# Kernel tuning notes

Hardware: AMD Instinct MI355X
Metric: run time of the kernel (lower is better)

## Reference

```python
import jax, jax.numpy as jnp
import numpy as np

N = 10000       # nodes
E = 320000      # edges
D = 256         # feature dim (out_channels)
L = 5           # num_layers


def setup_inputs() -> dict:
    key = jax.random.key(0)
    ks = jax.random.split(key, 8)
    x = jax.random.normal(ks[0], (N, D), dtype=jnp.float32)
    edge_index = jax.random.randint(ks[1], (2, E), 0, N, dtype=jnp.int64)
    edge_attr = jax.random.uniform(ks[2], (E,), dtype=jnp.float32)
    s = 1.0 / np.sqrt(D)
    # per-layer message transform weights [L, D, D]
    weight = jax.random.uniform(ks[3], (L, D, D), minval=-s, maxval=s, dtype=jnp.float32)
    # GRUCell parameters (torch layout: [3D, D] rows = r, z, n)
    w_ih = jax.random.uniform(ks[4], (3 * D, D), minval=-s, maxval=s, dtype=jnp.float32)
    w_hh = jax.random.uniform(ks[5], (3 * D, D), minval=-s, maxval=s, dtype=jnp.float32)
    b_ih = jax.random.uniform(ks[6], (3 * D,), minval=-s, maxval=s, dtype=jnp.float32)
    b_hh = jax.random.uniform(ks[7], (3 * D,), minval=-s, maxval=s, dtype=jnp.float32)
    return {"x": x, "edge_index": edge_index, "edge_attr": edge_attr,
            "weight": weight, "w_ih": w_ih, "w_hh": w_hh,
            "b_ih": b_ih, "b_hh": b_hh}


def _gru_cell(inp, h, w_ih, w_hh, b_ih, b_hh):
    # torch.nn.GRUCell math
    gi = inp @ w_ih.T + b_ih    # [N, 3D]
    gh = h @ w_hh.T + b_hh      # [N, 3D]
    i_r, i_z, i_n = jnp.split(gi, 3, axis=-1)
    h_r, h_z, h_n = jnp.split(gh, 3, axis=-1)
    r = jax.nn.sigmoid(i_r + h_r)
    z = jax.nn.sigmoid(i_z + h_z)
    n = jnp.tanh(i_n + r * h_n)
    return (1.0 - z) * n + z * h


def reference(x, edge_index, edge_attr, weight, w_ih, w_hh, b_ih, b_hh):
    src, dst = edge_index[0], edge_index[1]
    h = x
    for l in range(L):
        m = h @ weight[l]                                   # [N, D]
        msg = m[src] * edge_attr[:, None]                   # [E, D]
        agg = jax.ops.segment_sum(msg, dst, num_segments=N)  # [N, D]
        h = _gru_cell(agg, h, w_ih, w_hh, b_ih, b_hh)
    return h
```

## Files before the change

kernel.cpp:

```cpp
#include <hip/hip_runtime.h>
#include <hip/hip_bf16.h>

#define NN 10000
#define NPAD 10048
#define EE 320000
#define DD 256
#define LL 5

typedef __bf16 bf16x8 __attribute__((ext_vector_type(8)));
typedef float f32x4 __attribute__((ext_vector_type(4)));

__device__ __forceinline__ void gload_lds16(const void* g, void* l) {
    __builtin_amdgcn_global_load_lds(
        (const __attribute__((address_space(1))) void*)g,
        (__attribute__((address_space(3))) void*)l, 16, 0, 0);
}


__global__ void transpose_wb_k(const float* __restrict__ W, __bf16* __restrict__ Wt) {
    __shared__ float t[32][33];
    int l = blockIdx.z;
    int bx = blockIdx.x * 32;
    int by = blockIdx.y * 32;
    for (int i = threadIdx.y; i < 32; i += 8)
        t[i][threadIdx.x] = W[l * 65536 + (by + i) * DD + bx + threadIdx.x];
    __syncthreads();
    for (int i = threadIdx.y; i < 32; i += 8)
        Wt[l * 65536 + (bx + i) * DD + by + threadIdx.x] = (__bf16)t[threadIdx.x][i];
}

__global__ void prep_k(const float* __restrict__ w_ih, const float* __restrict__ w_hh,
                       const float* __restrict__ x,
                       __bf16* __restrict__ wihb, __bf16* __restrict__ whhb,
                       float* __restrict__ hb, __bf16* __restrict__ hbfA,
                       __bf16* __restrict__ hbfB, __bf16* __restrict__ mb,
                       __bf16* __restrict__ aggb, int* __restrict__ deg) {
    int i = blockIdx.x * blockDim.x + threadIdx.x;
    if (i < NN * DD) { float v = x[i]; hb[i] = v; hbfA[i] = (__bf16)v; }
    if (i < 768 * 256) { wihb[i] = (__bf16)w_ih[i]; whhb[i] = (__bf16)w_hh[i]; }
    if (i < (NPAD - NN) * DD) {
        hbfA[NN * DD + i] = (__bf16)0.f;
        hbfB[NN * DD + i] = (__bf16)0.f;
        mb[NN * DD + i] = (__bf16)0.f;
        aggb[NN * DD + i] = (__bf16)0.f;
    }
    if (i < NN) deg[i] = 0;
}

__global__ void hist_k(const int* __restrict__ dst, int* __restrict__ deg) {
    int e = blockIdx.x * blockDim.x + threadIdx.x;
    if (e < EE) atomicAdd(&deg[dst[e]], 1);
}

__global__ void scan_k(const int* __restrict__ deg, int* __restrict__ row_start,
                       int* __restrict__ cursor) {
    __shared__ int sums[1024];
    const int CH = 10;
    int t = threadIdx.x;
    int base = t * CH;
    int loc[CH];
    int s = 0;
#pragma unroll
    for (int i = 0; i < CH; i++) {
        int v = (base + i < NN) ? deg[base + i] : 0;
        loc[i] = s;
        s += v;
    }
    sums[t] = s;
    __syncthreads();
    for (int off = 1; off < 1024; off <<= 1) {
        int v = (t >= off) ? sums[t - off] : 0;
        __syncthreads();
        sums[t] += v;
        __syncthreads();
    }
    int pre = (t == 0) ? 0 : sums[t - 1];
#pragma unroll
    for (int i = 0; i < CH; i++) {
        int idx = base + i;
        if (idx < NN) {
            int v = pre + loc[i];
            row_start[idx] = v;
            cursor[idx] = v;
        }
    }
    if (t == 1023) row_start[NN] = sums[1023];
}

__global__ void fill_k(const int* __restrict__ ei, const float* __restrict__ attr,
                       int* __restrict__ cursor, int* __restrict__ ssrc,
                       float* __restrict__ sattr) {
    int e = blockIdx.x * blockDim.x + threadIdx.x;
    if (e < EE) {
        int dv = ei[EE + e];
        int p = atomicAdd(&cursor[dv], 1);
        ssrc[p] = ei[e];
        sattr[p] = attr[e];
    }
}


__global__ __launch_bounds__(256, 2)
void gemm_m_k(const __bf16* __restrict__ hbf, const __bf16* __restrict__ wt,
              __bf16* __restrict__ mout) {
    __shared__ __bf16 sA[2][64][32];
    __shared__ __bf16 sB[2][64][32];
    int tid = threadIdx.x;
    int wave = tid >> 6, lane = tid & 63;
    int ln = lane & 15, quad = lane >> 4;
    int rowBlock = blockIdx.x * 64;
    int colBlock = blockIdx.y * 64;
    int rowHalf = (wave >> 1) * 32;
    int colHalf = (wave & 1) * 32;
    int r4 = lane >> 2;
    int kb = (lane & 3) * 8;

    f32x4 acc[2][2] = {};

    for (int k0 = 0; k0 < DD; k0 += 64) {
        __syncthreads();
#pragma unroll
        for (int ii = 0; ii < 4; ii++) {
            int idx = wave * 4 + ii;
            int mat = idx >> 3;
            int rem = idx & 7;
            int sub = rem >> 2;
            int rg = rem & 3;
            const __bf16* src;
            __bf16* dst;
            if (mat == 0) {
                src = hbf + (size_t)(rowBlock + rg * 16 + r4) * DD + k0 + sub * 32 + kb;
                dst = &sA[sub][rg * 16][0];
            } else {
                src = wt + (size_t)(colBlock + rg * 16 + r4) * DD + k0 + sub * 32 + kb;
                dst = &sB[sub][rg * 16][0];
            }
            gload_lds16(src, dst);
        }
        __syncthreads();

#pragma unroll
        for (int sub = 0; sub < 2; sub++) {
            bf16x8 af[2], bf[2];
#pragma unroll
            for (int i = 0; i < 2; i++)
                af[i] = *(const bf16x8*)&sA[sub][rowHalf + i * 16 + ln][quad * 8];
#pragma unroll
            for (int cc = 0; cc < 2; cc++)
                bf[cc] = *(const bf16x8*)&sB[sub][colHalf + cc * 16 + ln][quad * 8];
#pragma unroll
            for (int nf = 0; nf < 2; nf++)
#pragma unroll
                for (int cc = 0; cc < 2; cc++)
                    acc[nf][cc] = __builtin_amdgcn_mfma_f32_16x16x32_bf16(af[nf], bf[cc], acc[nf][cc], 0, 0, 0);
        }
    }
#pragma unroll
    for (int nf = 0; nf < 2; nf++)
#pragma unroll
        for (int r = 0; r < 4; r++) {
            int n = rowBlock + rowHalf + nf * 16 + quad * 4 + r;
#pragma unroll
            for (int cc = 0; cc < 2; cc++) {
                int d = colBlock + colHalf + cc * 16 + ln;
                mout[(size_t)n * DD + d] = (__bf16)acc[nf][cc][r];
            }
        }
}


__global__ __launch_bounds__(256)
void aggregate_bf_k(const __bf16* __restrict__ m, const int* __restrict__ row_start,
                    const int* __restrict__ ssrc, const float* __restrict__ sattr,
                    __bf16* __restrict__ aggb) {
    __shared__ int sIdx[4][64];
    __shared__ float sAtt[4][64];
    int w = threadIdx.x >> 6, lane = threadIdx.x & 63;
    int n = blockIdx.x * 4 + w;
    int s0 = row_start[n], s1 = row_start[n + 1];
    int half = lane >> 5;
    int c8 = (lane & 31) * 8;

    float acc[8] = {0.f, 0.f, 0.f, 0.f, 0.f, 0.f, 0.f, 0.f};

    for (int base = s0; base < s1; base += 64) {
        int cnt = min(64, s1 - base);
        if (lane < cnt) {
            sIdx[w][lane] = ssrc[base + lane];
            sAtt[w][lane] = sattr[base + lane];
        }
        int t = 0;
        for (; t + 8 <= cnt; t += 8) {
#pragma unroll
            for (int u = 0; u < 4; u++) {
                int e = t + u * 2 + half;
                int s = sIdx[w][e];
                float ww = sAtt[w][e];
                bf16x8 v = *(const bf16x8*)(m + (size_t)s * DD + c8);
#pragma unroll
                for (int i = 0; i < 8; i++) acc[i] += (float)v[i] * ww;
            }
        }
        for (; t + 2 <= cnt; t += 2) {
            int e = t + half;
            int s = sIdx[w][e];
            float ww = sAtt[w][e];
            bf16x8 v = *(const bf16x8*)(m + (size_t)s * DD + c8);
#pragma unroll
            for (int i = 0; i < 8; i++) acc[i] += (float)v[i] * ww;
        }
        if (t < cnt && half == 0) {
            int s = sIdx[w][t];
            float ww = sAtt[w][t];
            bf16x8 v = *(const bf16x8*)(m + (size_t)s * DD + c8);
#pragma unroll
            for (int i = 0; i < 8; i++) acc[i] += (float)v[i] * ww;
        }
    }

#pragma unroll
    for (int i = 0; i < 8; i++) acc[i] += __shfl_xor(acc[i], 32, 64);

    if (half == 0) {
        bf16x8 o;
#pragma unroll
        for (int i = 0; i < 8; i++) o[i] = (__bf16)acc[i];
        *(bf16x8*)(aggb + (size_t)n * DD + c8) = o;
    }
}


__global__ __launch_bounds__(256, 2)
void gru_mfma_k(const __bf16* __restrict__ aggb, const __bf16* __restrict__ hbf,
                const float* __restrict__ hin,
                const __bf16* __restrict__ wih, const __bf16* __restrict__ whh,
                const float* __restrict__ b_ih, const float* __restrict__ b_hh,
                float* __restrict__ hout, __bf16* __restrict__ hbfout) {
    __shared__ __bf16 sA[2][64][32];
    __shared__ __bf16 sB[6][64][32];
    int tid = threadIdx.x;
    int wave = tid >> 6, lane = tid & 63;
    int ln = lane & 15, quad = lane >> 4;
    int nodeBlock = blockIdx.x * 64;
    int colBlock = blockIdx.y * 64;
    int nodeHalf = (wave >> 1) * 32;
    int colHalf = (wave & 1) * 32;
    int r4 = lane >> 2;
    int kb = (lane & 3) * 8;

    f32x4 acc[6][2][2] = {};

    for (int k0 = 0; k0 < DD; k0 += 32) {
        __syncthreads();
#pragma unroll
        for (int ii = 0; ii < 8; ii++) {
            int idx = wave * 8 + ii;
            const __bf16* src;
            __bf16* dst;
            if (idx < 8) {
                int s = idx >> 2;
                int rg = idx & 3;
                const __bf16* A = s ? hbf : aggb;
                src = A + (size_t)(nodeBlock + rg * 16 + r4) * DD + k0 + kb;
                dst = &sA[s][rg * 16][0];
            } else {
                int j = idx - 8;
                int g6 = j >> 2;
                int rg = j & 3;
                const __bf16* B = (g6 < 3) ? wih : whh;
                int brow = (g6 % 3) * 256 + colBlock + rg * 16 + r4;
                src = B + (size_t)brow * DD + k0 + kb;
                dst = &sB[g6][rg * 16][0];
            }
            gload_lds16(src, dst);
        }
        __syncthreads();

        bf16x8 aA[2], aH[2];
#pragma unroll
        for (int nf = 0; nf < 2; nf++) {
            aA[nf] = *(const bf16x8*)&sA[0][nodeHalf + nf * 16 + ln][quad * 8];
            aH[nf] = *(const bf16x8*)&sA[1][nodeHalf + nf * 16 + ln][quad * 8];
        }
#pragma unroll
        for (int g = 0; g < 3; g++) {
#pragma unroll
            for (int cc = 0; cc < 2; cc++) {
                bf16x8 bI = *(const bf16x8*)&sB[g][colHalf + cc * 16 + ln][quad * 8];
                bf16x8 bH = *(const bf16x8*)&sB[3 + g][colHalf + cc * 16 + ln][quad * 8];
#pragma unroll
                for (int nf = 0; nf < 2; nf++) {
                    acc[g][nf][cc] = __builtin_amdgcn_mfma_f32_16x16x32_bf16(aA[nf], bI, acc[g][nf][cc], 0, 0, 0);
                    acc[3 + g][nf][cc] = __builtin_amdgcn_mfma_f32_16x16x32_bf16(aH[nf], bH, acc[3 + g][nf][cc], 0, 0, 0);
                }
            }
        }
    }

#pragma unroll
    for (int nf = 0; nf < 2; nf++) {
#pragma unroll
        for (int r = 0; r < 4; r++) {
            int n = nodeBlock + nodeHalf + nf * 16 + quad * 4 + r;
            if (n >= NN) continue;
#pragma unroll
            for (int cc = 0; cc < 2; cc++) {
                int d = colBlock + colHalf + cc * 16 + ln;
                float ir = acc[0][nf][cc][r] + b_ih[d];
                float iz = acc[1][nf][cc][r] + b_ih[d + 256];
                float in_ = acc[2][nf][cc][r] + b_ih[d + 512];
                float hr = acc[3][nf][cc][r] + b_hh[d];
                float hz = acc[4][nf][cc][r] + b_hh[d + 256];
                float hn = acc[5][nf][cc][r] + b_hh[d + 512];
                float rr = 1.f / (1.f + __expf(-(ir + hr)));
                float zz = 1.f / (1.f + __expf(-(iz + hz)));
                float ax = in_ + rr * hn;
                float e2 = __expf(-2.f * ax);
                float nnv = 2.f / (1.f + e2) - 1.f;
                float hp = hin[(size_t)n * DD + d];
                float o = (1.f - zz) * nnv + zz * hp;
                hout[(size_t)n * DD + d] = o;
                hbfout[(size_t)n * DD + d] = (__bf16)o;
            }
        }
    }
}


extern "C" void kernel_launch(void* const* d_in, const int* in_sizes, int n_in,
                              void* d_out, int out_size, void* d_ws, size_t ws_size,
                              hipStream_t stream) {
    const float* x = (const float*)d_in[0];
    const int* edge_index = (const int*)d_in[1];
    const float* edge_attr = (const float*)d_in[2];
    const float* weight = (const float*)d_in[3];
    const float* w_ih = (const float*)d_in[4];
    const float* w_hh = (const float*)d_in[5];
    const float* b_ih = (const float*)d_in[6];
    const float* b_hh = (const float*)d_in[7];

    size_t off = 0;
    char* base = (char*)d_ws;
    auto carve = [&](size_t bytes) -> void* {
        void* p = base + off;
        off += (bytes + 255) & ~(size_t)255;
        return p;
    };
    float* hb = (float*)carve((size_t)NPAD * DD * 4);
    __bf16* hbfA = (__bf16*)carve((size_t)NPAD * DD * 2);
    __bf16* hbfB = (__bf16*)carve((size_t)NPAD * DD * 2);
    __bf16* mb = (__bf16*)carve((size_t)NPAD * DD * 2);
    __bf16* aggb = (__bf16*)carve((size_t)NPAD * DD * 2);
    __bf16* wtb = (__bf16*)carve((size_t)LL * DD * DD * 2);
    __bf16* wihb = (__bf16*)carve((size_t)768 * DD * 2);
    __bf16* whhb = (__bf16*)carve((size_t)768 * DD * 2);
    int* deg = (int*)carve((size_t)NN * 4);
    int* row_start = (int*)carve((size_t)(NN + 1) * 4);
    int* cursor = (int*)carve((size_t)NN * 4);
    int* ssrc = (int*)carve((size_t)EE * 4);
    float* sattr = (float*)carve((size_t)EE * 4);
    (void)ws_size;

    transpose_wb_k<<<dim3(8, 8, LL), dim3(32, 8), 0, stream>>>(weight, wtb);
    prep_k<<<(NN * DD + 255) / 256, 256, 0, stream>>>(w_ih, w_hh, x, wihb, whhb,
                                                      hb, hbfA, hbfB, mb, aggb, deg);
    hist_k<<<(EE + 255) / 256, 256, 0, stream>>>(edge_index + EE, deg);
    scan_k<<<1, 1024, 0, stream>>>(deg, row_start, cursor);
    fill_k<<<(EE + 255) / 256, 256, 0, stream>>>(edge_index, edge_attr, cursor, ssrc, sattr);

    float* hA = hb;
    float* hB = (float*)d_out;
    __bf16* hbfIn = hbfA;
    __bf16* hbfOut = hbfB;
    for (int l = 0; l < LL; l++) {
        gemm_m_k<<<dim3(157, 4), 256, 0, stream>>>(hbfIn, wtb + (size_t)l * DD * DD, mb);
        aggregate_bf_k<<<2500, 256, 0, stream>>>(mb, row_start, ssrc, sattr, aggb);
        gru_mfma_k<<<dim3(157, 4), 256, 0, stream>>>(aggb, hbfIn, hA, wihb, whhb,
                                                     b_ih, b_hh, hB, hbfOut);
        float* t = hA; hA = hB; hB = t;
        __bf16* tb = hbfIn; hbfIn = hbfOut; hbfOut = tb;
    }
}
```

Before: 371.5 us.

## Fold per-layer message weight into GRU input weights, drop message GEMM

Uses linearity: segment_sum((h@W_l)[src]*a) @ W_ih^T equals segment_sum(h[src]*a) @ (W_ih W_l^T)^T, so a fused weight W_ih·W_l^T is precomputed once per layer in fp32 and stored as bf16. The per-layer gemm_m_k launch and the m buffer go away, and aggregation reads h directly. The GRU GEMM's input-weight operand becomes the fused per-layer matrix. This trades a small one-time fp32 GEMM for five removed N×D×D GEMMs, and changes where bf16 rounding occurs, which alters numerics slightly.

New measurement: 352.1 us. -5.2%, faster.

```diff
diff --git a/kernel.cpp b/kernel.cpp
--- a/kernel.cpp
+++ b/kernel.cpp
@@ -8,6 +8,7 @@
 #define LL 5
 
 typedef __bf16 bf16x8 __attribute__((ext_vector_type(8)));
+typedef __bf16 bf16x4 __attribute__((ext_vector_type(4)));
 typedef float f32x4 __attribute__((ext_vector_type(4)));
 
 __device__ __forceinline__ void gload_lds16(const void* g, void* l) {
@@ -17,31 +18,17 @@
 }
 
 
-__global__ void transpose_wb_k(const float* __restrict__ W, __bf16* __restrict__ Wt) {
-    __shared__ float t[32][33];
-    int l = blockIdx.z;
-    int bx = blockIdx.x * 32;
-    int by = blockIdx.y * 32;
-    for (int i = threadIdx.y; i < 32; i += 8)
-        t[i][threadIdx.x] = W[l * 65536 + (by + i) * DD + bx + threadIdx.x];
-    __syncthreads();
-    for (int i = threadIdx.y; i < 32; i += 8)
-        Wt[l * 65536 + (bx + i) * DD + by + threadIdx.x] = (__bf16)t[threadIdx.x][i];
-}
-
-__global__ void prep_k(const float* __restrict__ w_ih, const float* __restrict__ w_hh,
-                       const float* __restrict__ x,
-                       __bf16* __restrict__ wihb, __bf16* __restrict__ whhb,
+__global__ void prep_k(const float* __restrict__ w_hh, const float* __restrict__ x,
+                       __bf16* __restrict__ whhb,
                        float* __restrict__ hb, __bf16* __restrict__ hbfA,
-                       __bf16* __restrict__ hbfB, __bf16* __restrict__ mb,
-                       __bf16* __restrict__ aggb, int* __restrict__ deg) {
+                       __bf16* __restrict__ hbfB, __bf16* __restrict__ aggb,
+                       int* __restrict__ deg) {
     int i = blockIdx.x * blockDim.x + threadIdx.x;
     if (i < NN * DD) { float v = x[i]; hb[i] = v; hbfA[i] = (__bf16)v; }
-    if (i < 768 * 256) { wihb[i] = (__bf16)w_ih[i]; whhb[i] = (__bf16)w_hh[i]; }
+    if (i < 768 * 256) whhb[i] = (__bf16)w_hh[i];
     if (i < (NPAD - NN) * DD) {
         hbfA[NN * DD + i] = (__bf16)0.f;
         hbfB[NN * DD + i] = (__bf16)0.f;
-        mb[NN * DD + i] = (__bf16)0.f;
         aggb[NN * DD + i] = (__bf16)0.f;
     }
     if (i < NN) deg[i] = 0;
@@ -100,77 +87,59 @@
 }
 
 
-__global__ __launch_bounds__(256, 2)
-void gemm_m_k(const __bf16* __restrict__ hbf, const __bf16* __restrict__ wt,
-              __bf16* __restrict__ mout) {
-    __shared__ __bf16 sA[2][64][32];
-    __shared__ __bf16 sB[2][64][32];
+__global__ __launch_bounds__(256)
+void beff32_k(const float* __restrict__ wih, const float* __restrict__ W,
+              __bf16* __restrict__ beff) {
+    __shared__ float As[16][68];
+    __shared__ float Bs[16][68];
+    int l = blockIdx.z;
+    const float* Wl = W + (size_t)l * DD * DD;
+    __bf16* Cl = beff + (size_t)l * 768 * DD;
     int tid = threadIdx.x;
-    int wave = tid >> 6, lane = tid & 63;
-    int ln = lane & 15, quad = lane >> 4;
-    int rowBlock = blockIdx.x * 64;
-    int colBlock = blockIdx.y * 64;
-    int rowHalf = (wave >> 1) * 32;
-    int colHalf = (wave & 1) * 32;
-    int r4 = lane >> 2;
-    int kb = (lane & 3) * 8;
-
-    f32x4 acc[2][2] = {};
-
-    for (int k0 = 0; k0 < DD; k0 += 64) {
-        __syncthreads();
-#pragma unroll
-        for (int ii = 0; ii < 4; ii++) {
-            int idx = wave * 4 + ii;
-            int mat = idx >> 3;
-            int rem = idx & 7;
-            int sub = rem >> 2;
-            int rg = rem & 3;
-            const __bf16* src;
-            __bf16* dst;
-            if (mat == 0) {
-                src = hbf + (size_t)(rowBlock + rg * 16 + r4) * DD + k0 + sub * 32 + kb;
-                dst = &sA[sub][rg * 16][0];
-            } else {
-                src = wt + (size_t)(colBlock + rg * 16 + r4) * DD + k0 + sub * 32 + kb;
-                dst = &sB[sub][rg * 16][0];
-            }
-            gload_lds16(src, dst);
-        }
-        __syncthreads();
-
-#pragma unroll
-        for (int sub = 0; sub < 2; sub++) {
-            bf16x8 af[2], bf[2];
-#pragma unroll
-            for (int i = 0; i < 2; i++)
-                af[i] = *(const bf16x8*)&sA[sub][rowHalf + i * 16 + ln][quad * 8];
-#pragma unroll
-            for (int cc = 0; cc < 2; cc++)
-                bf[cc] = *(const bf16x8*)&sB[sub][colHalf + cc * 16 + ln][quad * 8];
-#pragma unroll
-            for (int nf = 0; nf < 2; nf++)
-#pragma unroll
-                for (int cc = 0; cc < 2; cc++)
-                    acc[nf][cc] = __builtin_amdgcn_mfma_f32_16x16x32_bf16(af[nf], bf[cc], acc[nf][cc], 0, 0, 0);
-        }
-    }
-#pragma unroll
-    for (int nf = 0; nf < 2; nf++)
-#pragma unroll
-        for (int r = 0; r < 4; r++) {
-            int n = rowBlock + rowHalf + nf * 16 + quad * 4 + r;
-#pragma unroll
-            for (int cc = 0; cc < 2; cc++) {
-                int d = colBlock + colHalf + cc * 16 + ln;
-                mout[(size_t)n * DD + d] = (__bf16)acc[nf][cc][r];
-            }
-        }
+    int tx = tid & 15, ty = tid >> 4;
+    int jBase = blockIdx.x * 64;
+    int tBase = blockIdx.y * 64;
+    int lr = tid >> 2, lq = tid & 3;
+    float acc[4][4];
+#pragma unroll
+    for (int i = 0; i < 4; i++)
+#pragma unroll
+        for (int j = 0; j < 4; j++) acc[i][j] = 0.f;
+
+    for (int k0 = 0; k0 < DD; k0 += 16) {
+        float4 av = *(const float4*)(wih + (size_t)(jBase + lr) * DD + k0 + lq * 4);
+        float4 bv = *(const float4*)(Wl + (size_t)(tBase + lr) * DD + k0 + lq * 4);
+        __syncthreads();
+        As[lq * 4 + 0][lr] = av.x; As[lq * 4 + 1][lr] = av.y;
+        As[lq * 4 + 2][lr] = av.z; As[lq * 4 + 3][lr] = av.w;
+        Bs[lq * 4 + 0][lr] = bv.x; Bs[lq * 4 + 1][lr] = bv.y;
+        Bs[lq * 4 + 2][lr] = bv.z; Bs[lq * 4 + 3][lr] = bv.w;
+        __syncthreads();
+#pragma unroll
+        for (int kk = 0; kk < 16; kk++) {
+            float a0 = As[kk][ty * 4 + 0], a1 = As[kk][ty * 4 + 1];
+            float a2 = As[kk][ty * 4 + 2], a3 = As[kk][ty * 4 + 3];
+            float b0 = Bs[kk][tx * 4 + 0], b1 = Bs[kk][tx * 4 + 1];
+            float b2 = Bs[kk][tx * 4 + 2], b3 = Bs[kk][tx * 4 + 3];
+            acc[0][0] += a0 * b0; acc[0][1] += a0 * b1; acc[0][2] += a0 * b2; acc[0][3] += a0 * b3;
+            acc[1][0] += a1 * b0; acc[1][1] += a1 * b1; acc[1][2] += a1 * b2; acc[1][3] += a1 * b3;
+            acc[2][0] += a2 * b0; acc[2][1] += a2 * b1; acc[2][2] += a2 * b2; acc[2][3] += a2 * b3;
+            acc[3][0] += a3 * b0; acc[3][1] += a3 * b1; acc[3][2] += a3 * b2; acc[3][3] += a3 * b3;
+        }
+    }
+#pragma unroll
+    for (int i = 0; i < 4; i++) {
+        int j = jBase + ty * 4 + i;
+        bf16x4 o;
+        o[0] = (__bf16)acc[i][0]; o[1] = (__bf16)acc[i][1];
+        o[2] = (__bf16)acc[i][2]; o[3] = (__bf16)acc[i][3];
+        *(bf16x4*)(Cl + (size_t)j * DD + tBase + tx * 4) = o;
+    }
 }
 
 
 __global__ __launch_bounds__(256)
-void aggregate_bf_k(const __bf16* __restrict__ m, const int* __restrict__ row_start,
+void aggregate_bf_k(const __bf16* __restrict__ hsrc, const int* __restrict__ row_start,
                     const int* __restrict__ ssrc, const float* __restrict__ sattr,
                     __bf16* __restrict__ aggb) {
     __shared__ int sIdx[4][64];
@@ -196,7 +165,7 @@
                 int e = t + u * 2 + half;
                 int s = sIdx[w][e];
                 float ww = sAtt[w][e];
-                bf16x8 v = *(const bf16x8*)(m + (size_t)s * DD + c8);
+                bf16x8 v = *(const bf16x8*)(hsrc + (size_t)s * DD + c8);
 #pragma unroll
                 for (int i = 0; i < 8; i++) acc[i] += (float)v[i] * ww;
             }
@@ -205,14 +174,14 @@
             int e = t + half;
             int s = sIdx[w][e];
             float ww = sAtt[w][e];
-            bf16x8 v = *(const bf16x8*)(m + (size_t)s * DD + c8);
+            bf16x8 v = *(const bf16x8*)(hsrc + (size_t)s * DD + c8);
 #pragma unroll
             for (int i = 0; i < 8; i++) acc[i] += (float)v[i] * ww;
         }
         if (t < cnt && half == 0) {
             int s = sIdx[w][t];
             float ww = sAtt[w][t];
-            bf16x8 v = *(const bf16x8*)(m + (size_t)s * DD + c8);
+            bf16x8 v = *(const bf16x8*)(hsrc + (size_t)s * DD + c8);
 #pragma unroll
             for (int i = 0; i < 8; i++) acc[i] += (float)v[i] * ww;
         }
@@ -233,7 +202,7 @@
 __global__ __launch_bounds__(256, 2)
 void gru_mfma_k(const __bf16* __restrict__ aggb, const __bf16* __restrict__ hbf,
                 const float* __restrict__ hin,
-                const __bf16* __restrict__ wih, const __bf16* __restrict__ whh,
+                const __bf16* __restrict__ bihw, const __bf16* __restrict__ whh,
                 const float* __restrict__ b_ih, const float* __restrict__ b_hh,
                 float* __restrict__ hout, __bf16* __restrict__ hbfout) {
     __shared__ __bf16 sA[2][64][32];
@@ -267,7 +236,7 @@
                 int j = idx - 8;
                 int g6 = j >> 2;
                 int rg = j & 3;
-                const __bf16* B = (g6 < 3) ? wih : whh;
+                const __bf16* B = (g6 < 3) ? bihw : whh;
                 int brow = (g6 % 3) * 256 + colBlock + rg * 16 + r4;
                 src = B + (size_t)brow * DD + k0 + kb;
                 dst = &sB[g6][rg * 16][0];
@@ -349,11 +318,9 @@
     float* hb = (float*)carve((size_t)NPAD * DD * 4);
     __bf16* hbfA = (__bf16*)carve((size_t)NPAD * DD * 2);
     __bf16* hbfB = (__bf16*)carve((size_t)NPAD * DD * 2);
-    __bf16* mb = (__bf16*)carve((size_t)NPAD * DD * 2);
     __bf16* aggb = (__bf16*)carve((size_t)NPAD * DD * 2);
-    __bf16* wtb = (__bf16*)carve((size_t)LL * DD * DD * 2);
-    __bf16* wihb = (__bf16*)carve((size_t)768 * DD * 2);
     __bf16* whhb = (__bf16*)carve((size_t)768 * DD * 2);
+    __bf16* beff = (__bf16*)carve((size_t)LL * 768 * DD * 2);
     int* deg = (int*)carve((size_t)NN * 4);
     int* row_start = (int*)carve((size_t)(NN + 1) * 4);
     int* cursor = (int*)carve((size_t)NN * 4);
@@ -361,21 +328,21 @@
     float* sattr = (float*)carve((size_t)EE * 4);
     (void)ws_size;
 
-    transpose_wb_k<<<dim3(8, 8, LL), dim3(32, 8), 0, stream>>>(weight, wtb);
-    prep_k<<<(NN * DD + 255) / 256, 256, 0, stream>>>(w_ih, w_hh, x, wihb, whhb,
-                                                      hb, hbfA, hbfB, mb, aggb, deg);
+    prep_k<<<(NN * DD + 255) / 256, 256, 0, stream>>>(w_hh, x, whhb, hb, hbfA, hbfB,
+                                                      aggb, deg);
     hist_k<<<(EE + 255) / 256, 256, 0, stream>>>(edge_index + EE, deg);
     scan_k<<<1, 1024, 0, stream>>>(deg, row_start, cursor);
     fill_k<<<(EE + 255) / 256, 256, 0, stream>>>(edge_index, edge_attr, cursor, ssrc, sattr);
+    beff32_k<<<dim3(12, 4, LL), 256, 0, stream>>>(w_ih, weight, beff);
 
     float* hA = hb;
     float* hB = (float*)d_out;
     __bf16* hbfIn = hbfA;
     __bf16* hbfOut = hbfB;
     for (int l = 0; l < LL; l++) {
-        gemm_m_k<<<dim3(157, 4), 256, 0, stream>>>(hbfIn, wtb + (size_t)l * DD * DD, mb);
-        aggregate_bf_k<<<2500, 256, 0, stream>>>(mb, row_start, ssrc, sattr, aggb);
-        gru_mfma_k<<<dim3(157, 4), 256, 0, stream>>>(aggb, hbfIn, hA, wihb, whhb,
+        aggregate_bf_k<<<2500, 256, 0, stream>>>(hbfIn, row_start, ssrc, sattr, aggb);
+        gru_mfma_k<<<dim3(157, 4), 256, 0, stream>>>(aggb, hbfIn, hA,
+                                                     beff + (size_t)l * 768 * DD, whhb,
                                                      b_ih, b_hh, hB, hbfOut);
         float* t = hA; hA = hB; hB = t;
         __bf16* tb = hbfIn; hbfIn = hbfOut; hbfOut = tb;
```
